# Performance work log

Hardware: AMD Instinct MI355X
Metric: run time of the kernel (lower is better)

Reference implementation:

```python
import jax, jax.numpy as jnp
import numpy as np

B, T, H, K = 128, 4096, 128, 5


def logistic_logcdf(x, mean, log_scale):
    z = (x - mean) * jnp.exp(-log_scale)
    return jax.nn.log_sigmoid(z)


def logistic_logpdf(x, mean, log_scale):
    z = (x - mean) * jnp.exp(-log_scale)
    zh = z / 2
    return -2 * jnp.logaddexp(zh, -zh) - log_scale


def mixlogistic_logcdf(x, prior_logits, means, log_scales):
    x = x[..., None]
    log_pi = jax.nn.log_softmax(prior_logits, axis=-1)
    return jax.nn.logsumexp(log_pi + logistic_logcdf(x, means, log_scales), axis=-1)


def mixlogistic_logpdf(x, prior_logits, means, log_scales):
    x = x[..., None]
    log_pi = jax.nn.log_softmax(prior_logits, axis=-1)
    return jax.nn.logsumexp(log_pi + logistic_logpdf(x, means, log_scales), axis=-1)


def coupling_function(x, pi, mu, log_s):
    log_cdf = jnp.minimum(mixlogistic_logcdf(x, pi, mu, log_s), -1e-12)
    log_1m = jnp.log(-jnp.expm1(log_cdf))
    val = log_cdf - log_1m
    log_jac = mixlogistic_logpdf(x, pi, mu, log_s) - log_cdf - log_1m
    return val, log_jac


def gru_step(h, x, Wi, Wh, bi, bhn):
    # flax GRUCell: input denses have bias, hidden denses no bias except hn.
    gi = x @ Wi + bi                      # [B, 3H]
    gh = h @ Wh                           # [B, 3H]
    ir, iz, inn = jnp.split(gi, 3, axis=-1)
    hr, hz, hn = jnp.split(gh, 3, axis=-1)
    r = jax.nn.sigmoid(ir + hr)
    z = jax.nn.sigmoid(iz + hz)
    n = jnp.tanh(inn + r * (hn + bhn))
    return (1.0 - z) * n + z * h


def setup_inputs() -> dict:
    key = jax.random.key(0)
    ks = jax.random.split(key, 14)
    g = lambda i, shape: (jax.random.normal(ks[i], shape) * 0.08).astype(jnp.float32)
    return {
        's': jax.random.normal(ks[0], (B, T), jnp.float32),
        'x': jax.random.normal(ks[1], (B, T), jnp.float32),
        'eps': jax.random.logistic(ks[2], (B, T), jnp.float32),
        # encoder GRU (in_features=1)
        'Wi_e': g(3, (1, 3 * H)), 'Wh_e': g(4, (H, 3 * H)),
        'bi_e': jnp.zeros(3 * H, jnp.float32), 'bhn_e': jnp.zeros(H, jnp.float32),
        # decoder GRU (in_features=1+H)
        'Wi_d': g(5, (1 + H, 3 * H)), 'Wh_d': g(6, (H, 3 * H)),
        'bi_d': jnp.zeros(3 * H, jnp.float32), 'bhn_d': jnp.zeros(H, jnp.float32),
        # heads
        'W_shift': g(7, (H, 1)), 'b_shift': jnp.zeros(1, jnp.float32),
        'W_lsc': g(8, (H, 1)), 'b_lsc': jnp.zeros(1, jnp.float32),
        'W_pi': g(9, (H, K)), 'b_pi': jnp.zeros(K, jnp.float32),
        'W_mu': g(10, (H, K)), 'b_mu': jnp.zeros(K, jnp.float32),
        'W_ls': g(11, (H, K)), 'b_ls': jnp.zeros(K, jnp.float32),
    }


def reference(s, x, eps, Wi_e, Wh_e, bi_e, bhn_e, Wi_d, Wh_d, bi_d, bhn_d,
              W_shift, b_shift, W_lsc, b_lsc, W_pi, b_pi, W_mu, b_mu, W_ls, b_ls):
    Bn, Tn = s.shape
    Hn = Wh_e.shape[0]
    s3 = s[..., None]  # [B,T,1]
    x3 = x[..., None]

    # --- encoder: reverse GRU, outputs kept in scan (reversed) order ---
    def enc_step(h, xt):
        h = gru_step(h, xt, Wi_e, Wh_e, bi_e, bhn_e)
        return h, h

    x_rev = jnp.flip(x3, axis=1).transpose(1, 0, 2)  # [T,B,1]
    _, h_x = jax.lax.scan(enc_step, jnp.zeros((Bn, Hn), s.dtype), x_rev)
    h_x = h_x.transpose(1, 0, 2)  # [B,T,H]

    sc = jnp.concatenate([s3, h_x], axis=-1)  # [B,T,1+H]

    def dec_step(carry, xs_t):
        h, pred = carry
        inp, e = xs_t              # inp [B,1+H], e [B]
        inp = inp.at[:, 0].set(pred)
        h = gru_step(h, inp, Wi_d, Wh_d, bi_d, bhn_d)
        y = h
        shift = (y @ W_shift + b_shift)[:, 0]
        log_scale = (y @ W_lsc + b_lsc)[:, 0]
        pi = y @ W_pi + b_pi
        mu = y @ W_mu + b_mu
        log_s = y @ W_ls + b_ls
        val, log_jac = coupling_function(e, pi, mu, log_s)
        prediction = shift + val * jnp.exp(log_scale)
        # standard logistic logpdf(e) = -e - 2*softplus(-e)
        logp = (-e - 2 * jax.nn.softplus(-e)) - log_scale - log_jac
        return (h, prediction), (logp, prediction)

    carry0 = (jnp.zeros((Bn, Hn), s.dtype), jnp.zeros(Bn, s.dtype))
    xs = (sc.transpose(1, 0, 2), eps.T)
    _, (logp, preds) = jax.lax.scan(dec_step, carry0, xs)
    return logp.T, preds.T  # each [B,T]
```

## Files before the change

### kernel.cpp

```cpp
#include <hip/hip_runtime.h>
#include <hip/hip_fp16.h>

#define Tn 4096
#define Bn 128
#define Hn 128
#define G3 384
#define NTH 192

typedef unsigned short u16;
typedef unsigned int u32;
typedef _Float16 f16;
typedef _Float16 h2 __attribute__((ext_vector_type(2)));

__device__ __forceinline__ float sigm(float v) { return 1.f / (1.f + __expf(-v)); }
__device__ __forceinline__ float tanh_fast(float v) {
  v = fminf(fmaxf(v, -15.f), 15.f);
  float e = __expf(-2.f * v);
  return (1.f - e) / (1.f + e);
}
__device__ __forceinline__ u16 f2h(float f) { return __half_as_ushort(__float2half(f)); }
__device__ __forceinline__ float h2f(u16 u) { return __half2float(__ushort_as_half(u)); }
__device__ __forceinline__ h2 bch2(u32 v) { union { u32 u; h2 h; } t; t.u = v; return t.h; }
__device__ __forceinline__ float fdot2f(h2 a, h2 b, float c) {
  return __builtin_amdgcn_fdot2(a, b, c, false);
}

__global__ __launch_bounds__(NTH, 1) void combo_kernel(
    const float* __restrict__ x, const float* __restrict__ Wi_e,
    const float* __restrict__ Wh_e, const float* __restrict__ bi_e,
    const float* __restrict__ bhn_e, u16* __restrict__ hx,
    float* __restrict__ enc_h,
    const float* __restrict__ eps, const float* __restrict__ Wi_d,
    const float* __restrict__ Wh_d, const float* __restrict__ bhn_d,
    const float* __restrict__ W_shift, const float* __restrict__ b_shift,
    const float* __restrict__ W_lsc, const float* __restrict__ b_lsc,
    const float* __restrict__ W_pi, const float* __restrict__ b_pi,
    const float* __restrict__ W_mu, const float* __restrict__ b_mu,
    const float* __restrict__ W_ls, const float* __restrict__ b_ls,
    const u16* __restrict__ gi2, float* __restrict__ out,
    float* __restrict__ dec_h, float* __restrict__ dec_pred,
    int enc_t0, int dec_t0, int Tc)
{
  const int j = threadIdx.x;
  __shared__ __align__(16) f16 Xp[2][Hn];
  __shared__ float pred_s;
  const int bid = blockIdx.x;
  int cur = 0;

  if (bid < Bn) {
    if (enc_t0 < 0) return;
    const int b = bid, t0 = enc_t0;
    h2 wr_[64], wz_[64], wn_[64];
    float wieR = 0, wieZ = 0, wieN = 0, bieR = 0, bieZ = 0, bieN = 0;
    float bhn = 0, hm = 0;
    if (j < Hn) {
#pragma unroll
      for (int q = 0; q < 64; ++q) {
        h2 a, bq, c;
        a.x = (f16)Wh_e[(2 * q) * G3 + j];        a.y = (f16)Wh_e[(2 * q + 1) * G3 + j];
        bq.x = (f16)Wh_e[(2 * q) * G3 + 128 + j]; bq.y = (f16)Wh_e[(2 * q + 1) * G3 + 128 + j];
        c.x = (f16)Wh_e[(2 * q) * G3 + 256 + j];  c.y = (f16)Wh_e[(2 * q + 1) * G3 + 256 + j];
        wr_[q] = a; wz_[q] = bq; wn_[q] = c;
      }
      wieR = Wi_e[j]; wieZ = Wi_e[128 + j]; wieN = Wi_e[256 + j];
      bieR = bi_e[j]; bieZ = bi_e[128 + j]; bieN = bi_e[256 + j];
      bhn = bhn_e[j];
      hm = (t0 == 0) ? 0.f : enc_h[(long)b * Hn + j];
      Xp[0][j] = (f16)hm;
    }
    __syncthreads();
    const float* xrow = x + (long)b * Tn;
    u16* hxrow = hx + ((long)b * Hn + (j < Hn ? j : 0)) * Tc;
    for (int i8 = 0; i8 < Tc; i8 += 8) {
      float xc0 = 0, xc1 = 0, xc2 = 0, xc3 = 0, xc4 = 0, xc5 = 0, xc6 = 0, xc7 = 0;
      u32 hb0 = 0, hb1 = 0, hb2 = 0, hb3 = 0;
      if (j < Hn) {
        int base = Tn - 8 - t0 - i8; if (base < 0) base = 0;
        float4 v0 = *(const float4*)(xrow + base);
        float4 v1 = *(const float4*)(xrow + base + 4);
        xc0 = v1.w; xc1 = v1.z; xc2 = v1.y; xc3 = v1.x;
        xc4 = v0.w; xc5 = v0.z; xc6 = v0.y; xc7 = v0.x;
      }
#pragma unroll
      for (int u = 0; u < 8; ++u) {
        if (j < Hn) {
          const uint4* hp = (const uint4*)Xp[cur];
          float a0r = 0, a1r = 0, a0z = 0, a1z = 0, a0n = 0, a1n = 0;
#pragma unroll
          for (int q = 0; q < 16; ++q) {
            uint4 hv = hp[q];
            a0r = fdot2f(bch2(hv.x), wr_[4 * q + 0], a0r);
            a1r = fdot2f(bch2(hv.y), wr_[4 * q + 1], a1r);
            a0r = fdot2f(bch2(hv.z), wr_[4 * q + 2], a0r);
            a1r = fdot2f(bch2(hv.w), wr_[4 * q + 3], a1r);
            a0z = fdot2f(bch2(hv.x), wz_[4 * q + 0], a0z);
            a1z = fdot2f(bch2(hv.y), wz_[4 * q + 1], a1z);
            a0z = fdot2f(bch2(hv.z), wz_[4 * q + 2], a0z);
            a1z = fdot2f(bch2(hv.w), wz_[4 * q + 3], a1z);
            a0n = fdot2f(bch2(hv.x), wn_[4 * q + 0], a0n);
            a1n = fdot2f(bch2(hv.y), wn_[4 * q + 1], a1n);
            a0n = fdot2f(bch2(hv.z), wn_[4 * q + 2], a0n);
            a1n = fdot2f(bch2(hv.w), wn_[4 * q + 3], a1n);
          }
          const float xt = (u == 0) ? xc0 : (u == 1) ? xc1 : (u == 2) ? xc2
                          : (u == 3) ? xc3 : (u == 4) ? xc4 : (u == 5) ? xc5
                          : (u == 6) ? xc6 : xc7;
          float r = sigm((a0r + a1r) + fmaf(xt, wieR, bieR));
          float z = sigm((a0z + a1z) + fmaf(xt, wieZ, bieZ));
          float n = tanh_fast(fmaf(xt, wieN, bieN) + r * ((a0n + a1n) + bhn));
          hm = (1.f - z) * n + z * hm;
          Xp[cur ^ 1][j] = (f16)hm;
          u16 hv16 = f2h(hm);
          if (u == 0) hb0 = hv16; else if (u == 1) hb0 |= ((u32)hv16 << 16);
          else if (u == 2) hb1 = hv16; else if (u == 3) hb1 |= ((u32)hv16 << 16);
          else if (u == 4) hb2 = hv16; else if (u == 5) hb2 |= ((u32)hv16 << 16);
          else if (u == 6) hb3 = hv16; else hb3 |= ((u32)hv16 << 16);
        }
        __syncthreads();
        cur ^= 1;
      }
      if (j < Hn) {
        uint4 o; o.x = hb0; o.y = hb1; o.z = hb2; o.w = hb3;
        *(uint4*)(hxrow + i8) = o;
      }
    }
    if (j < Hn) enc_h[(long)b * Hn + j] = hm;
  } else {
    if (dec_t0 < 0) return;
    const int b = bid - Bn, t0 = dec_t0;
    const int lane = j - 128;
    h2 wr_[64], wz_[64], wn_[64];
    h2 wp2[32];
    float wr0 = 0, wz0 = 0, wn0 = 0, bhn = 0, hm = 0;
    float hbias = 0, predreg = 0;
    if (j < Hn) {
#pragma unroll
      for (int q = 0; q < 64; ++q) {
        h2 a, bq, c;
        a.x = (f16)Wh_d[(2 * q) * G3 + j];        a.y = (f16)Wh_d[(2 * q + 1) * G3 + j];
        bq.x = (f16)Wh_d[(2 * q) * G3 + 128 + j]; bq.y = (f16)Wh_d[(2 * q + 1) * G3 + 128 + j];
        c.x = (f16)Wh_d[(2 * q) * G3 + 256 + j];  c.y = (f16)Wh_d[(2 * q + 1) * G3 + 256 + j];
        wr_[q] = a; wz_[q] = bq; wn_[q] = c;
      }
      wr0 = Wi_d[j]; wz0 = Wi_d[128 + j]; wn0 = Wi_d[256 + j];
      bhn = bhn_d[j];
      hm = (t0 == 0) ? 0.f : dec_h[(long)b * Hn + j];
      Xp[0][j] = (f16)hm;
    } else {
      const int ho = lane >> 1, hs = lane & 1;
      if (lane < 34) {
#pragma unroll
        for (int q = 0; q < 32; ++q) {
          int ka = 2 * (hs * 32 + q), kb = ka + 1;
          float wa, wb;
          if (ho == 0) { wa = W_shift[ka]; wb = W_shift[kb]; }
          else if (ho == 1) { wa = W_lsc[ka]; wb = W_lsc[kb]; }
          else if (ho < 7) { wa = W_pi[ka * 5 + ho - 2]; wb = W_pi[kb * 5 + ho - 2]; }
          else if (ho < 12) { wa = W_mu[ka * 5 + ho - 7]; wb = W_mu[kb * 5 + ho - 7]; }
          else { wa = W_ls[ka * 5 + ho - 12]; wb = W_ls[kb * 5 + ho - 12]; }
          h2 t; t.x = (f16)wa; t.y = (f16)wb;
          wp2[q] = t;
        }
        hbias = (ho == 0) ? b_shift[0] : (ho == 1) ? b_lsc[0] : (ho < 7) ? b_pi[ho - 2]
              : (ho < 12) ? b_mu[ho - 7] : b_ls[ho - 12];
      } else {
#pragma unroll
        for (int q = 0; q < 32; ++q) { h2 t; t.x = (f16)0.f; t.y = (f16)0.f; wp2[q] = t; }
      }
      predreg = (t0 == 0) ? 0.f : dec_pred[b];
      if (lane == 0) pred_s = predreg;
    }
    const float* erow = eps + (long)b * Tn;
    const u16* gibase = gi2 + (long)b * G3 * Tc;
    float ep = 0.f;
    float lp0 = 0, lp1 = 0, lp2 = 0, lp3 = 0, lp4 = 0, lp5 = 0, lp6 = 0, lp7 = 0;
    float pr0 = 0, pr1 = 0, pr2 = 0, pr3 = 0, pr4 = 0, pr5 = 0, pr6 = 0, pr7 = 0;
    float* outlp = out + (long)b * Tn + t0;
    float* outpr = out + (long)Bn * Tn + (long)b * Tn + t0;
    __syncthreads();

    auto couple = [&](float e, const f16* Xc) -> float2 {
      const int hs = lane & 1;
      float p = 0.f;
      if (lane < 34) {
        const uint4* hp4 = (const uint4*)Xc;
#pragma unroll
        for (int q = 0; q < 8; ++q) {
          uint4 hv = hp4[hs * 8 + q];
          p = fdot2f(bch2(hv.x), wp2[4 * q + 0], p);
          p = fdot2f(bch2(hv.y), wp2[4 * q + 1], p);
          p = fdot2f(bch2(hv.z), wp2[4 * q + 2], p);
          p = fdot2f(bch2(hv.w), wp2[4 * q + 3], p);
        }
      }
      p += __shfl_xor(p, 1);
      float pb = p + hbias;
      const int lj2 = lane & 7;
      float pi_ = __shfl(pb, 4 + 2 * lj2);
      float mu_ = __shfl(pb, 14 + 2 * lj2);
      float ls_ = __shfl(pb, 24 + 2 * lj2);
      float shiftv = __shfl(pb, 0);
      float lscv = __shfl(pb, 2);
      const bool valid = (lane < 5);
      float wexp = valid ? __expf(pi_) : 0.f;
      float zz = (e - mu_) * __expf(-ls_);
      float uq = __expf(-fabsf(zz));
      float dq = 1.f / (1.f + uq);
      float sigp = (zz >= 0.f) ? dq : uq * dq;
      float sigq = (zz >= 0.f) ? uq * dq : dq;
      float pdfl = uq * dq * dq * __expf(-ls_);
      float c = wexp * sigp, m = wexp * sigq, pq = wexp * pdfl, S = wexp;
      c += __shfl_xor(c, 1, 8); m += __shfl_xor(m, 1, 8);
      pq += __shfl_xor(pq, 1, 8); S += __shfl_xor(S, 1, 8);
      c += __shfl_xor(c, 2, 8); m += __shfl_xor(m, 2, 8);
      pq += __shfl_xor(pq, 2, 8); S += __shfl_xor(S, 2, 8);
      c += __shfl_xor(c, 4, 8); m += __shfl_xor(m, 4, 8);
      pq += __shfl_xor(pq, 4, 8); S += __shfl_xor(S, 4, 8);
      float logc = __logf(c), logm = __logf(m);
      float val = logc - logm;
      float ljac = __logf(pq) + __logf(S) - logc - logm;
      float prednew = fmaf(val, __expf(lscv), shiftv);
      float sp = fmaxf(-e, 0.f) + log1pf(__expf(-fabsf(e)));
      float logp = (-e - 2.f * sp) - lscv - ljac;
      return make_float2(logp, prednew);
    };

    for (int i8 = 0; i8 < Tc; i8 += 8) {
      uint4 gR4 = {0, 0, 0, 0}, gZ4 = {0, 0, 0, 0}, gN4 = {0, 0, 0, 0};
      float ec0 = 0, ec1 = 0, ec2 = 0, ec3 = 0, ec4 = 0, ec5 = 0, ec6 = 0, ec7 = 0;
      if (j < Hn) {
        gR4 = *(const uint4*)(gibase + (long)j * Tc + i8);
        gZ4 = *(const uint4*)(gibase + (long)(128 + j) * Tc + i8);
        gN4 = *(const uint4*)(gibase + (long)(256 + j) * Tc + i8);
      } else {
        float4 v0 = *(const float4*)(erow + t0 + i8);
        float4 v1 = *(const float4*)(erow + t0 + i8 + 4);
        ec0 = v0.x; ec1 = v0.y; ec2 = v0.z; ec3 = v0.w;
        ec4 = v1.x; ec5 = v1.y; ec6 = v1.z; ec7 = v1.w;
      }
#pragma unroll
      for (int u = 0; u < 8; ++u) {
        const int i = i8 + u;
        float ar = 0, az = 0, an = 0;
        if (j < Hn) {
          const uint4* hp = (const uint4*)Xp[cur];
          float a0r = 0, a1r = 0, a0z = 0, a1z = 0, a0n = 0, a1n = 0;
#pragma unroll
          for (int q = 0; q < 16; ++q) {
            uint4 hv = hp[q];
            a0r = fdot2f(bch2(hv.x), wr_[4 * q + 0], a0r);
            a1r = fdot2f(bch2(hv.y), wr_[4 * q + 1], a1r);
            a0r = fdot2f(bch2(hv.z), wr_[4 * q + 2], a0r);
            a1r = fdot2f(bch2(hv.w), wr_[4 * q + 3], a1r);
            a0z = fdot2f(bch2(hv.x), wz_[4 * q + 0], a0z);
            a1z = fdot2f(bch2(hv.y), wz_[4 * q + 1], a1z);
            a0z = fdot2f(bch2(hv.z), wz_[4 * q + 2], a0z);
            a1z = fdot2f(bch2(hv.w), wz_[4 * q + 3], a1z);
            a0n = fdot2f(bch2(hv.x), wn_[4 * q + 0], a0n);
            a1n = fdot2f(bch2(hv.y), wn_[4 * q + 1], a1n);
            a0n = fdot2f(bch2(hv.z), wn_[4 * q + 2], a0n);
            a1n = fdot2f(bch2(hv.w), wn_[4 * q + 3], a1n);
          }
          ar = a0r + a1r; az = a0z + a1z; an = a0n + a1n;
        } else if (i >= 1) {
          float e = (u == 0) ? ep : (u == 1) ? ec0 : (u == 2) ? ec1 : (u == 3) ? ec2
                  : (u == 4) ? ec3 : (u == 5) ? ec4 : (u == 6) ? ec5 : ec6;
          float2 rr = couple(e, Xp[cur]);
          if (lane == 0) {
            if (u == 0) { lp7 = rr.x; pr7 = rr.y; }
            else if (u == 1) { lp0 = rr.x; pr0 = rr.y; }
            else if (u == 2) { lp1 = rr.x; pr1 = rr.y; }
            else if (u == 3) { lp2 = rr.x; pr2 = rr.y; }
            else if (u == 4) { lp3 = rr.x; pr3 = rr.y; }
            else if (u == 5) { lp4 = rr.x; pr4 = rr.y; }
            else if (u == 6) { lp5 = rr.x; pr5 = rr.y; }
            else { lp6 = rr.x; pr6 = rr.y; }
            pred_s = rr.y;
            predreg = rr.y;
            if (u == 0 && i8 > 0) {
              *(float4*)(outlp + i8 - 8) = make_float4(lp0, lp1, lp2, lp3);
              *(float4*)(outlp + i8 - 4) = make_float4(lp4, lp5, lp6, lp7);
              *(float4*)(outpr + i8 - 8) = make_float4(pr0, pr1, pr2, pr3);
              *(float4*)(outpr + i8 - 4) = make_float4(pr4, pr5, pr6, pr7);
            }
          }
        }
        __syncthreads();
        if (j < Hn) {
          u16 gvr = (u == 0) ? (u16)gR4.x : (u == 1) ? (u16)(gR4.x >> 16)
                  : (u == 2) ? (u16)gR4.y : (u == 3) ? (u16)(gR4.y >> 16)
                  : (u == 4) ? (u16)gR4.z : (u == 5) ? (u16)(gR4.z >> 16)
                  : (u == 6) ? (u16)gR4.w : (u16)(gR4.w >> 16);
          u16 gvz = (u == 0) ? (u16)gZ4.x : (u == 1) ? (u16)(gZ4.x >> 16)
                  : (u == 2) ? (u16)gZ4.y : (u == 3) ? (u16)(gZ4.y >> 16)
                  : (u == 4) ? (u16)gZ4.z : (u == 5) ? (u16)(gZ4.z >> 16)
                  : (u == 6) ? (u16)gZ4.w : (u16)(gZ4.w >> 16);
          u16 gvn = (u == 0) ? (u16)gN4.x : (u == 1) ? (u16)(gN4.x >> 16)
                  : (u == 2) ? (u16)gN4.y : (u == 3) ? (u16)(gN4.y >> 16)
                  : (u == 4) ? (u16)gN4.z : (u == 5) ? (u16)(gN4.z >> 16)
                  : (u == 6) ? (u16)gN4.w : (u16)(gN4.w >> 16);
          float pred = pred_s;
          float r = sigm(ar + h2f(gvr) + pred * wr0);
          float z = sigm(az + h2f(gvz) + pred * wz0);
          float n = tanh_fast(h2f(gvn) + pred * wn0 + r * (an + bhn));
          hm = (1.f - z) * n + z * hm;
          Xp[cur ^ 1][j] = (f16)hm;
        }
        __syncthreads();
        cur ^= 1;
      }
      if (j >= 128) ep = ec7;
    }
    if (j >= 128) {
      float2 rr = couple(ep, Xp[cur]);
      if (lane == 0) {
        lp7 = rr.x; pr7 = rr.y; predreg = rr.y;
        *(float4*)(outlp + Tc - 8) = make_float4(lp0, lp1, lp2, lp3);
        *(float4*)(outlp + Tc - 4) = make_float4(lp4, lp5, lp6, lp7);
        *(float4*)(outpr + Tc - 8) = make_float4(pr0, pr1, pr2, pr3);
        *(float4*)(outpr + Tc - 4) = make_float4(pr4, pr5, pr6, pr7);
      }
    }
    if (j < Hn) dec_h[(long)b * Hn + j] = hm;
    if (j == 128) dec_pred[b] = predreg;
  }
}

__global__ __launch_bounds__(256) void gemm_gi(
    const u16* __restrict__ A2, const float* __restrict__ Wi_d,
    const float* __restrict__ bi_d, u16* __restrict__ C2, int Tc)
{
  __shared__ __align__(16) float As[16][64];
  __shared__ __align__(16) float Ws[16][64];
  const int tid = threadIdx.x;
  const long m0 = (long)blockIdx.x * 64;
  const int n0 = blockIdx.y * 64;
  const int bb = (int)(m0 / Tc);
  const int tt0 = (int)(m0 - (long)bb * Tc);
  const int tx = tid & 15, ty = tid >> 4;
  const int lk = tid >> 4, lm = (tid & 15) * 4;
  const int wk = tid >> 4, wn = (tid & 15) * 4;
  float acc[4][4] = {};
  for (int k0 = 0; k0 < Hn; k0 += 16) {
    uint2 a2v = *(const uint2*)(A2 + ((long)bb * Hn + k0 + lk) * Tc + tt0 + lm);
    float4 w4 = *(const float4*)(Wi_d + (long)(1 + k0 + wk) * G3 + n0 + wn);
    __syncthreads();
    As[lk][lm + 0] = h2f((u16)(a2v.x & 0xffffu));
    As[lk][lm + 1] = h2f((u16)(a2v.x >> 16));
    As[lk][lm + 2] = h2f((u16)(a2v.y & 0xffffu));
    As[lk][lm + 3] = h2f((u16)(a2v.y >> 16));
    *(float4*)&Ws[wk][wn] = w4;
    __syncthreads();
#pragma unroll
    for (int kk = 0; kk < 16; ++kk) {
      float4 av = *(const float4*)&As[kk][ty * 4];
      float4 wv = *(const float4*)&Ws[kk][tx * 4];
      float ar[4] = {av.x, av.y, av.z, av.w};
      float wr[4] = {wv.x, wv.y, wv.z, wv.w};
#pragma unroll
      for (int i = 0; i < 4; ++i)
#pragma unroll
        for (int jj = 0; jj < 4; ++jj) acc[i][jj] = fmaf(ar[i], wr[jj], acc[i][jj]);
    }
  }
  const float4 bbv = *(const float4*)(bi_d + n0 + tx * 4);
  const float br[4] = {bbv.x, bbv.y, bbv.z, bbv.w};
#pragma unroll
  for (int jj = 0; jj < 4; ++jj) {
    int colc = n0 + tx * 4 + jj;
    u32 lo = (u32)f2h(acc[0][jj] + br[jj]) | ((u32)f2h(acc[1][jj] + br[jj]) << 16);
    u32 hi = (u32)f2h(acc[2][jj] + br[jj]) | ((u32)f2h(acc[3][jj] + br[jj]) << 16);
    uint2 o; o.x = lo; o.y = hi;
    *(uint2*)(C2 + ((long)bb * G3 + colc) * Tc + tt0 + ty * 4) = o;
  }
}

extern "C" void kernel_launch(void* const* d_in, const int* in_sizes, int n_in,
                              void* d_out, int out_size, void* d_ws, size_t ws_size,
                              hipStream_t stream) {
  const float* x = (const float*)d_in[1];
  const float* eps = (const float*)d_in[2];
  const float* Wi_e = (const float*)d_in[3];
  const float* Wh_e = (const float*)d_in[4];
  const float* bi_e = (const float*)d_in[5];
  const float* bhn_e = (const float*)d_in[6];
  const float* Wi_d = (const float*)d_in[7];
  const float* Wh_d = (const float*)d_in[8];
  const float* bi_d = (const float*)d_in[9];
  const float* bhn_d = (const float*)d_in[10];
  const float* W_shift = (const float*)d_in[11];
  const float* b_shift = (const float*)d_in[12];
  const float* W_lsc = (const float*)d_in[13];
  const float* b_lsc = (const float*)d_in[14];
  const float* W_pi = (const float*)d_in[15];
  const float* b_pi = (const float*)d_in[16];
  const float* W_mu = (const float*)d_in[17];
  const float* b_mu = (const float*)d_in[18];
  const float* W_ls = (const float*)d_in[19];
  const float* b_ls = (const float*)d_in[20];
  float* out = (float*)d_out;

  const size_t stateB = (size_t)(2 * Bn * Hn + Bn) * sizeof(float);
  const size_t stateAl = (stateB + 255) & ~(size_t)255;
  int Tc = 512;
  while (Tc > 64 && stateAl + (size_t)Bn * Tc * (Hn + G3) * 2 > ws_size) Tc >>= 1;
  if (stateAl + (size_t)Bn * Tc * (Hn + G3) * 2 > ws_size) return;

  float* enc_h = (float*)d_ws;
  float* dec_h = enc_h + (size_t)Bn * Hn;
  float* dec_pred = dec_h + (size_t)Bn * Hn;
  u16* hx = (u16*)((char*)d_ws + stateAl);
  u16* gi = hx + (size_t)Bn * Tc * Hn;

  const int Nc = Tn / Tc;
  const dim3 gg((unsigned)(((size_t)Bn * Tc) / 64), G3 / 64);
  for (int k = 0; k <= Nc; ++k) {
    int enc_t0 = (k < Nc) ? k * Tc : -1;
    int dec_t0 = (k >= 1) ? (k - 1) * Tc : -1;
    combo_kernel<<<2 * Bn, NTH, 0, stream>>>(
        x, Wi_e, Wh_e, bi_e, bhn_e, hx, enc_h,
        eps, Wi_d, Wh_d, bhn_d, W_shift, b_shift, W_lsc, b_lsc,
        W_pi, b_pi, W_mu, b_mu, W_ls, b_ls,
        gi, out, dec_h, dec_pred, enc_t0, dec_t0, Tc);
    if (k < Nc) gemm_gi<<<gg, 256, 0, stream>>>(hx, Wi_d, bi_d, gi, Tc);
  }
}
```

Before: 5.693 ms.

## Split GRU recurrent matvec across an extra wave computing the n-gate

Adds a fourth wavefront per block that computes the candidate-gate (n) hidden matvec and passes it through shared memory, so the main 128 threads handle only the r and z gates. This shortens the serial per-timestep dot-product chain and cuts per-thread weight registers from three gate arrays to two. The head/coupling lane moves to the new fourth wave, and encoder and decoder blocks now share one unified code path. The cost is an extra shared-memory round trip per step and more threads taking part in each barrier.

```diff
diff --git a/kernel.cpp b/kernel.cpp
--- a/kernel.cpp
+++ b/kernel.cpp
@@ -5,7 +5,7 @@
 #define Bn 128
 #define Hn 128
 #define G3 384
-#define NTH 192
+#define NTH 256
 
 typedef unsigned short u16;
 typedef unsigned int u32;
@@ -43,250 +43,232 @@
 {
   const int j = threadIdx.x;
   __shared__ __align__(16) f16 Xp[2][Hn];
+  __shared__ __align__(16) float nds[Hn];
   __shared__ float pred_s;
   const int bid = blockIdx.x;
   int cur = 0;
-
-  if (bid < Bn) {
-    if (enc_t0 < 0) return;
-    const int b = bid, t0 = enc_t0;
-    h2 wr_[64], wz_[64], wn_[64];
-    float wieR = 0, wieZ = 0, wieN = 0, bieR = 0, bieZ = 0, bieN = 0;
-    float bhn = 0, hm = 0;
-    if (j < Hn) {
-#pragma unroll
-      for (int q = 0; q < 64; ++q) {
-        h2 a, bq, c;
-        a.x = (f16)Wh_e[(2 * q) * G3 + j];        a.y = (f16)Wh_e[(2 * q + 1) * G3 + j];
-        bq.x = (f16)Wh_e[(2 * q) * G3 + 128 + j]; bq.y = (f16)Wh_e[(2 * q + 1) * G3 + 128 + j];
-        c.x = (f16)Wh_e[(2 * q) * G3 + 256 + j];  c.y = (f16)Wh_e[(2 * q + 1) * G3 + 256 + j];
-        wr_[q] = a; wz_[q] = bq; wn_[q] = c;
-      }
+  const bool is_enc = bid < Bn;
+  if (is_enc) { if (enc_t0 < 0) return; } else { if (dec_t0 < 0) return; }
+  const int b = is_enc ? bid : bid - Bn;
+  const int t0 = is_enc ? enc_t0 : dec_t0;
+  const float* Wh = is_enc ? Wh_e : Wh_d;
+
+  h2 wa_[64], wb_[64];
+  float hm = 0.f;
+  float bhn = 0, wr0 = 0, wz0 = 0, wn0 = 0;
+  float wieR = 0, wieZ = 0, wieN = 0, bieR = 0, bieZ = 0, bieN = 0;
+  h2 wp2[32];
+  float hbias = 0, predreg = 0;
+
+  if (j < Hn) {
+#pragma unroll
+    for (int q = 0; q < 64; ++q) {
+      h2 a, bq;
+      a.x = (f16)Wh[(2 * q) * G3 + j];        a.y = (f16)Wh[(2 * q + 1) * G3 + j];
+      bq.x = (f16)Wh[(2 * q) * G3 + 128 + j]; bq.y = (f16)Wh[(2 * q + 1) * G3 + 128 + j];
+      wa_[q] = a; wb_[q] = bq;
+    }
+    if (is_enc) {
       wieR = Wi_e[j]; wieZ = Wi_e[128 + j]; wieN = Wi_e[256 + j];
       bieR = bi_e[j]; bieZ = bi_e[128 + j]; bieN = bi_e[256 + j];
       bhn = bhn_e[j];
       hm = (t0 == 0) ? 0.f : enc_h[(long)b * Hn + j];
-      Xp[0][j] = (f16)hm;
-    }
-    __syncthreads();
-    const float* xrow = x + (long)b * Tn;
-    u16* hxrow = hx + ((long)b * Hn + (j < Hn ? j : 0)) * Tc;
-    for (int i8 = 0; i8 < Tc; i8 += 8) {
-      float xc0 = 0, xc1 = 0, xc2 = 0, xc3 = 0, xc4 = 0, xc5 = 0, xc6 = 0, xc7 = 0;
-      u32 hb0 = 0, hb1 = 0, hb2 = 0, hb3 = 0;
-      if (j < Hn) {
+    } else {
+      wr0 = Wi_d[j]; wz0 = Wi_d[128 + j]; wn0 = Wi_d[256 + j];
+      bhn = bhn_d[j];
+      hm = (t0 == 0) ? 0.f : dec_h[(long)b * Hn + j];
+    }
+    Xp[0][j] = (f16)hm;
+  } else if (j < 192) {
+    const int l = j - 128;
+#pragma unroll
+    for (int q = 0; q < 64; ++q) {
+      h2 a, bq;
+      a.x = (f16)Wh[(2 * q) * G3 + 256 + 2 * l];
+      a.y = (f16)Wh[(2 * q + 1) * G3 + 256 + 2 * l];
+      bq.x = (f16)Wh[(2 * q) * G3 + 256 + 2 * l + 1];
+      bq.y = (f16)Wh[(2 * q + 1) * G3 + 256 + 2 * l + 1];
+      wa_[q] = a; wb_[q] = bq;
+    }
+  } else if (!is_enc) {
+    const int lane = j - 192, ho = lane >> 1, hs = lane & 1;
+    if (lane < 34) {
+#pragma unroll
+      for (int q = 0; q < 32; ++q) {
+        int ka = 2 * (hs * 32 + q), kb = ka + 1;
+        float wva, wvb;
+        if (ho == 0) { wva = W_shift[ka]; wvb = W_shift[kb]; }
+        else if (ho == 1) { wva = W_lsc[ka]; wvb = W_lsc[kb]; }
+        else if (ho < 7) { wva = W_pi[ka * 5 + ho - 2]; wvb = W_pi[kb * 5 + ho - 2]; }
+        else if (ho < 12) { wva = W_mu[ka * 5 + ho - 7]; wvb = W_mu[kb * 5 + ho - 7]; }
+        else { wva = W_ls[ka * 5 + ho - 12]; wvb = W_ls[kb * 5 + ho - 12]; }
+        h2 t; t.x = (f16)wva; t.y = (f16)wvb;
+        wp2[q] = t;
+      }
+      hbias = (ho == 0) ? b_shift[0] : (ho == 1) ? b_lsc[0] : (ho < 7) ? b_pi[ho - 2]
+            : (ho < 12) ? b_mu[ho - 7] : b_ls[ho - 12];
+    } else {
+#pragma unroll
+      for (int q = 0; q < 32; ++q) { h2 t; t.x = (f16)0.f; t.y = (f16)0.f; wp2[q] = t; }
+    }
+    predreg = (t0 == 0) ? 0.f : dec_pred[b];
+    if (lane == 0) pred_s = predreg;
+  }
+  __syncthreads();
+
+  const float* xrow = x + (long)b * Tn;
+  const float* erow = eps + (long)b * Tn;
+  const u16* gibase = gi2 + (long)b * G3 * Tc;
+  u16* hxrow = hx + ((long)b * Hn + (j < Hn ? j : 0)) * Tc;
+  float* outlp = out + (long)b * Tn + t0;
+  float* outpr = out + (long)Bn * Tn + (long)b * Tn + t0;
+  const int lane3 = j - 192;
+  float ep = 0.f;
+  float lp0 = 0, lp1 = 0, lp2 = 0, lp3 = 0, lp4 = 0, lp5 = 0, lp6 = 0, lp7 = 0;
+  float pr0 = 0, pr1 = 0, pr2 = 0, pr3 = 0, pr4 = 0, pr5 = 0, pr6 = 0, pr7 = 0;
+
+  auto couple = [&](float e, const f16* Xc) -> float2 {
+    const int hs = lane3 & 1;
+    float p = 0.f;
+    if (lane3 < 34) {
+      const uint4* hp4 = (const uint4*)Xc;
+#pragma unroll
+      for (int q = 0; q < 8; ++q) {
+        uint4 hv = hp4[hs * 8 + q];
+        p = fdot2f(bch2(hv.x), wp2[4 * q + 0], p);
+        p = fdot2f(bch2(hv.y), wp2[4 * q + 1], p);
+        p = fdot2f(bch2(hv.z), wp2[4 * q + 2], p);
+        p = fdot2f(bch2(hv.w), wp2[4 * q + 3], p);
+      }
+    }
+    p += __shfl_xor(p, 1);
+    float pb = p + hbias;
+    const int lj2 = lane3 & 7;
+    float pi_ = __shfl(pb, 4 + 2 * lj2);
+    float mu_ = __shfl(pb, 14 + 2 * lj2);
+    float ls_ = __shfl(pb, 24 + 2 * lj2);
+    float shiftv = __shfl(pb, 0);
+    float lscv = __shfl(pb, 2);
+    const bool valid = (lane3 < 5);
+    float wexp = valid ? __expf(pi_) : 0.f;
+    float zz = (e - mu_) * __expf(-ls_);
+    float uq = __expf(-fabsf(zz));
+    float dq = 1.f / (1.f + uq);
+    float sigp = (zz >= 0.f) ? dq : uq * dq;
+    float sigq = (zz >= 0.f) ? uq * dq : dq;
+    float pdfl = uq * dq * dq * __expf(-ls_);
+    float c = wexp * sigp, m = wexp * sigq, pq = wexp * pdfl, S = wexp;
+    c += __shfl_xor(c, 1, 8); m += __shfl_xor(m, 1, 8);
+    pq += __shfl_xor(pq, 1, 8); S += __shfl_xor(S, 1, 8);
+    c += __shfl_xor(c, 2, 8); m += __shfl_xor(m, 2, 8);
+    pq += __shfl_xor(pq, 2, 8); S += __shfl_xor(S, 2, 8);
+    c += __shfl_xor(c, 4, 8); m += __shfl_xor(m, 4, 8);
+    pq += __shfl_xor(pq, 4, 8); S += __shfl_xor(S, 4, 8);
+    float logc = __logf(c), logm = __logf(m);
+    float val = logc - logm;
+    float ljac = __logf(pq) + __logf(S) - logc - logm;
+    float prednew = fmaf(val, __expf(lscv), shiftv);
+    float sp = fmaxf(-e, 0.f) + log1pf(__expf(-fabsf(e)));
+    float logp = (-e - 2.f * sp) - lscv - ljac;
+    return make_float2(logp, prednew);
+  };
+
+  for (int i8 = 0; i8 < Tc; i8 += 8) {
+    uint4 gR4 = {0, 0, 0, 0}, gZ4 = {0, 0, 0, 0}, gN4 = {0, 0, 0, 0};
+    float xc0 = 0, xc1 = 0, xc2 = 0, xc3 = 0, xc4 = 0, xc5 = 0, xc6 = 0, xc7 = 0;
+    float ec0 = 0, ec1 = 0, ec2 = 0, ec3 = 0, ec4 = 0, ec5 = 0, ec6 = 0, ec7 = 0;
+    u32 hb0 = 0, hb1 = 0, hb2 = 0, hb3 = 0;
+    if (j < Hn) {
+      if (is_enc) {
         int base = Tn - 8 - t0 - i8; if (base < 0) base = 0;
         float4 v0 = *(const float4*)(xrow + base);
         float4 v1 = *(const float4*)(xrow + base + 4);
         xc0 = v1.w; xc1 = v1.z; xc2 = v1.y; xc3 = v1.x;
         xc4 = v0.w; xc5 = v0.z; xc6 = v0.y; xc7 = v0.x;
+      } else {
+        gR4 = *(const uint4*)(gibase + (long)j * Tc + i8);
+        gZ4 = *(const uint4*)(gibase + (long)(128 + j) * Tc + i8);
+        gN4 = *(const uint4*)(gibase + (long)(256 + j) * Tc + i8);
       }
-#pragma unroll
-      for (int u = 0; u < 8; ++u) {
-        if (j < Hn) {
-          const uint4* hp = (const uint4*)Xp[cur];
-          float a0r = 0, a1r = 0, a0z = 0, a1z = 0, a0n = 0, a1n = 0;
-#pragma unroll
-          for (int q = 0; q < 16; ++q) {
-            uint4 hv = hp[q];
-            a0r = fdot2f(bch2(hv.x), wr_[4 * q + 0], a0r);
-            a1r = fdot2f(bch2(hv.y), wr_[4 * q + 1], a1r);
-            a0r = fdot2f(bch2(hv.z), wr_[4 * q + 2], a0r);
-            a1r = fdot2f(bch2(hv.w), wr_[4 * q + 3], a1r);
-            a0z = fdot2f(bch2(hv.x), wz_[4 * q + 0], a0z);
-            a1z = fdot2f(bch2(hv.y), wz_[4 * q + 1], a1z);
-            a0z = fdot2f(bch2(hv.z), wz_[4 * q + 2], a0z);
-            a1z = fdot2f(bch2(hv.w), wz_[4 * q + 3], a1z);
-            a0n = fdot2f(bch2(hv.x), wn_[4 * q + 0], a0n);
-            a1n = fdot2f(bch2(hv.y), wn_[4 * q + 1], a1n);
-            a0n = fdot2f(bch2(hv.z), wn_[4 * q + 2], a0n);
-            a1n = fdot2f(bch2(hv.w), wn_[4 * q + 3], a1n);
+    } else if (j >= 192 && !is_enc) {
+      float4 v0 = *(const float4*)(erow + t0 + i8);
+      float4 v1 = *(const float4*)(erow + t0 + i8 + 4);
+      ec0 = v0.x; ec1 = v0.y; ec2 = v0.z; ec3 = v0.w;
+      ec4 = v1.x; ec5 = v1.y; ec6 = v1.z; ec7 = v1.w;
+    }
+#pragma unroll
+    for (int u = 0; u < 8; ++u) {
+      const int i = i8 + u;
+      float ar = 0, az = 0;
+      if (j < Hn) {
+        const uint4* hp = (const uint4*)Xp[cur];
+        float a0r = 0, a1r = 0, a0z = 0, a1z = 0;
+#pragma unroll
+        for (int q = 0; q < 16; ++q) {
+          uint4 hv = hp[q];
+          a0r = fdot2f(bch2(hv.x), wa_[4 * q + 0], a0r);
+          a1r = fdot2f(bch2(hv.y), wa_[4 * q + 1], a1r);
+          a0r = fdot2f(bch2(hv.z), wa_[4 * q + 2], a0r);
+          a1r = fdot2f(bch2(hv.w), wa_[4 * q + 3], a1r);
+          a0z = fdot2f(bch2(hv.x), wb_[4 * q + 0], a0z);
+          a1z = fdot2f(bch2(hv.y), wb_[4 * q + 1], a1z);
+          a0z = fdot2f(bch2(hv.z), wb_[4 * q + 2], a0z);
+          a1z = fdot2f(bch2(hv.w), wb_[4 * q + 3], a1z);
+        }
+        ar = a0r + a1r; az = a0z + a1z;
+      } else if (j < 192) {
+        const int l = j - 128;
+        const uint4* hp = (const uint4*)Xp[cur];
+        float a0 = 0, a1 = 0, b0 = 0, b1 = 0;
+#pragma unroll
+        for (int q = 0; q < 16; ++q) {
+          uint4 hv = hp[q];
+          a0 = fdot2f(bch2(hv.x), wa_[4 * q + 0], a0);
+          a1 = fdot2f(bch2(hv.y), wa_[4 * q + 1], a1);
+          a0 = fdot2f(bch2(hv.z), wa_[4 * q + 2], a0);
+          a1 = fdot2f(bch2(hv.w), wa_[4 * q + 3], a1);
+          b0 = fdot2f(bch2(hv.x), wb_[4 * q + 0], b0);
+          b1 = fdot2f(bch2(hv.y), wb_[4 * q + 1], b1);
+          b0 = fdot2f(bch2(hv.z), wb_[4 * q + 2], b0);
+          b1 = fdot2f(bch2(hv.w), wb_[4 * q + 3], b1);
+        }
+        float2 nv; nv.x = a0 + a1; nv.y = b0 + b1;
+        *(float2*)&nds[2 * l] = nv;
+      } else if (!is_enc && i >= 1) {
+        float e = (u == 0) ? ep : (u == 1) ? ec0 : (u == 2) ? ec1 : (u == 3) ? ec2
+                : (u == 4) ? ec3 : (u == 5) ? ec4 : (u == 6) ? ec5 : ec6;
+        float2 rr = couple(e, Xp[cur]);
+        if (lane3 == 0) {
+          if (u == 0) { lp7 = rr.x; pr7 = rr.y; }
+          else if (u == 1) { lp0 = rr.x; pr0 = rr.y; }
+          else if (u == 2) { lp1 = rr.x; pr1 = rr.y; }
+          else if (u == 3) { lp2 = rr.x; pr2 = rr.y; }
+          else if (u == 4) { lp3 = rr.x; pr3 = rr.y; }
+          else if (u == 5) { lp4 = rr.x; pr4 = rr.y; }
+          else if (u == 6) { lp5 = rr.x; pr5 = rr.y; }
+          else { lp6 = rr.x; pr6 = rr.y; }
+          pred_s = rr.y;
+          predreg = rr.y;
+          if (u == 0 && i8 > 0) {
+            *(float4*)(outlp + i8 - 8) = make_float4(lp0, lp1, lp2, lp3);
+            *(float4*)(outlp + i8 - 4) = make_float4(lp4, lp5, lp6, lp7);
+            *(float4*)(outpr + i8 - 8) = make_float4(pr0, pr1, pr2, pr3);
+            *(float4*)(outpr + i8 - 4) = make_float4(pr4, pr5, pr6, pr7);
           }
+        }
+      }
+      __syncthreads();
+      if (j < Hn) {
+        float nd = nds[j];
+        float gir, giz, gin;
+        if (is_enc) {
           const float xt = (u == 0) ? xc0 : (u == 1) ? xc1 : (u == 2) ? xc2
                           : (u == 3) ? xc3 : (u == 4) ? xc4 : (u == 5) ? xc5
                           : (u == 6) ? xc6 : xc7;
-          float r = sigm((a0r + a1r) + fmaf(xt, wieR, bieR));
-          float z = sigm((a0z + a1z) + fmaf(xt, wieZ, bieZ));
-          float n = tanh_fast(fmaf(xt, wieN, bieN) + r * ((a0n + a1n) + bhn));
-          hm = (1.f - z) * n + z * hm;
-          Xp[cur ^ 1][j] = (f16)hm;
-          u16 hv16 = f2h(hm);
-          if (u == 0) hb0 = hv16; else if (u == 1) hb0 |= ((u32)hv16 << 16);
-          else if (u == 2) hb1 = hv16; else if (u == 3) hb1 |= ((u32)hv16 << 16);
-          else if (u == 4) hb2 = hv16; else if (u == 5) hb2 |= ((u32)hv16 << 16);
-          else if (u == 6) hb3 = hv16; else hb3 |= ((u32)hv16 << 16);
-        }
-        __syncthreads();
-        cur ^= 1;
-      }
-      if (j < Hn) {
-        uint4 o; o.x = hb0; o.y = hb1; o.z = hb2; o.w = hb3;
-        *(uint4*)(hxrow + i8) = o;
-      }
-    }
-    if (j < Hn) enc_h[(long)b * Hn + j] = hm;
-  } else {
-    if (dec_t0 < 0) return;
-    const int b = bid - Bn, t0 = dec_t0;
-    const int lane = j - 128;
-    h2 wr_[64], wz_[64], wn_[64];
-    h2 wp2[32];
-    float wr0 = 0, wz0 = 0, wn0 = 0, bhn = 0, hm = 0;
-    float hbias = 0, predreg = 0;
-    if (j < Hn) {
-#pragma unroll
-      for (int q = 0; q < 64; ++q) {
-        h2 a, bq, c;
-        a.x = (f16)Wh_d[(2 * q) * G3 + j];        a.y = (f16)Wh_d[(2 * q + 1) * G3 + j];
-        bq.x = (f16)Wh_d[(2 * q) * G3 + 128 + j]; bq.y = (f16)Wh_d[(2 * q + 1) * G3 + 128 + j];
-        c.x = (f16)Wh_d[(2 * q) * G3 + 256 + j];  c.y = (f16)Wh_d[(2 * q + 1) * G3 + 256 + j];
-        wr_[q] = a; wz_[q] = bq; wn_[q] = c;
-      }
-      wr0 = Wi_d[j]; wz0 = Wi_d[128 + j]; wn0 = Wi_d[256 + j];
-      bhn = bhn_d[j];
-      hm = (t0 == 0) ? 0.f : dec_h[(long)b * Hn + j];
-      Xp[0][j] = (f16)hm;
-    } else {
-      const int ho = lane >> 1, hs = lane & 1;
-      if (lane < 34) {
-#pragma unroll
-        for (int q = 0; q < 32; ++q) {
-          int ka = 2 * (hs * 32 + q), kb = ka + 1;
-          float wa, wb;
-          if (ho == 0) { wa = W_shift[ka]; wb = W_shift[kb]; }
-          else if (ho == 1) { wa = W_lsc[ka]; wb = W_lsc[kb]; }
-          else if (ho < 7) { wa = W_pi[ka * 5 + ho - 2]; wb = W_pi[kb * 5 + ho - 2]; }
-          else if (ho < 12) { wa = W_mu[ka * 5 + ho - 7]; wb = W_mu[kb * 5 + ho - 7]; }
-          else { wa = W_ls[ka * 5 + ho - 12]; wb = W_ls[kb * 5 + ho - 12]; }
-          h2 t; t.x = (f16)wa; t.y = (f16)wb;
-          wp2[q] = t;
-        }
-        hbias = (ho == 0) ? b_shift[0] : (ho == 1) ? b_lsc[0] : (ho < 7) ? b_pi[ho - 2]
-              : (ho < 12) ? b_mu[ho - 7] : b_ls[ho - 12];
-      } else {
-#pragma unroll
-        for (int q = 0; q < 32; ++q) { h2 t; t.x = (f16)0.f; t.y = (f16)0.f; wp2[q] = t; }
-      }
-      predreg = (t0 == 0) ? 0.f : dec_pred[b];
-      if (lane == 0) pred_s = predreg;
-    }
-    const float* erow = eps + (long)b * Tn;
-    const u16* gibase = gi2 + (long)b * G3 * Tc;
-    float ep = 0.f;
-    float lp0 = 0, lp1 = 0, lp2 = 0, lp3 = 0, lp4 = 0, lp5 = 0, lp6 = 0, lp7 = 0;
-    float pr0 = 0, pr1 = 0, pr2 = 0, pr3 = 0, pr4 = 0, pr5 = 0, pr6 = 0, pr7 = 0;
-    float* outlp = out + (long)b * Tn + t0;
-    float* outpr = out + (long)Bn * Tn + (long)b * Tn + t0;
-    __syncthreads();
-
-    auto couple = [&](float e, const f16* Xc) -> float2 {
-      const int hs = lane & 1;
-      float p = 0.f;
-      if (lane < 34) {
-        const uint4* hp4 = (const uint4*)Xc;
-#pragma unroll
-        for (int q = 0; q < 8; ++q) {
-          uint4 hv = hp4[hs * 8 + q];
-          p = fdot2f(bch2(hv.x), wp2[4 * q + 0], p);
-          p = fdot2f(bch2(hv.y), wp2[4 * q + 1], p);
-          p = fdot2f(bch2(hv.z), wp2[4 * q + 2], p);
-          p = fdot2f(bch2(hv.w), wp2[4 * q + 3], p);
-        }
-      }
-      p += __shfl_xor(p, 1);
-      float pb = p + hbias;
-      const int lj2 = lane & 7;
-      float pi_ = __shfl(pb, 4 + 2 * lj2);
-      float mu_ = __shfl(pb, 14 + 2 * lj2);
-      float ls_ = __shfl(pb, 24 + 2 * lj2);
-      float shiftv = __shfl(pb, 0);
-      float lscv = __shfl(pb, 2);
-      const bool valid = (lane < 5);
-      float wexp = valid ? __expf(pi_) : 0.f;
-      float zz = (e - mu_) * __expf(-ls_);
-      float uq = __expf(-fabsf(zz));
-      float dq = 1.f / (1.f + uq);
-      float sigp = (zz >= 0.f) ? dq : uq * dq;
-      float sigq = (zz >= 0.f) ? uq * dq : dq;
-      float pdfl = uq * dq * dq * __expf(-ls_);
-      float c = wexp * sigp, m = wexp * sigq, pq = wexp * pdfl, S = wexp;
-      c += __shfl_xor(c, 1, 8); m += __shfl_xor(m, 1, 8);
-      pq += __shfl_xor(pq, 1, 8); S += __shfl_xor(S, 1, 8);
-      c += __shfl_xor(c, 2, 8); m += __shfl_xor(m, 2, 8);
-      pq += __shfl_xor(pq, 2, 8); S += __shfl_xor(S, 2, 8);
-      c += __shfl_xor(c, 4, 8); m += __shfl_xor(m, 4, 8);
-      pq += __shfl_xor(pq, 4, 8); S += __shfl_xor(S, 4, 8);
-      float logc = __logf(c), logm = __logf(m);
-      float val = logc - logm;
-      float ljac = __logf(pq) + __logf(S) - logc - logm;
-      float prednew = fmaf(val, __expf(lscv), shiftv);
-      float sp = fmaxf(-e, 0.f) + log1pf(__expf(-fabsf(e)));
-      float logp = (-e - 2.f * sp) - lscv - ljac;
-      return make_float2(logp, prednew);
-    };
-
-    for (int i8 = 0; i8 < Tc; i8 += 8) {
-      uint4 gR4 = {0, 0, 0, 0}, gZ4 = {0, 0, 0, 0}, gN4 = {0, 0, 0, 0};
-      float ec0 = 0, ec1 = 0, ec2 = 0, ec3 = 0, ec4 = 0, ec5 = 0, ec6 = 0, ec7 = 0;
-      if (j < Hn) {
-        gR4 = *(const uint4*)(gibase + (long)j * Tc + i8);
-        gZ4 = *(const uint4*)(gibase + (long)(128 + j) * Tc + i8);
-        gN4 = *(const uint4*)(gibase + (long)(256 + j) * Tc + i8);
-      } else {
-        float4 v0 = *(const float4*)(erow + t0 + i8);
-        float4 v1 = *(const float4*)(erow + t0 + i8 + 4);
-        ec0 = v0.x; ec1 = v0.y; ec2 = v0.z; ec3 = v0.w;
-        ec4 = v1.x; ec5 = v1.y; ec6 = v1.z; ec7 = v1.w;
-      }
-#pragma unroll
-      for (int u = 0; u < 8; ++u) {
-        const int i = i8 + u;
-        float ar = 0, az = 0, an = 0;
-        if (j < Hn) {
-          const uint4* hp = (const uint4*)Xp[cur];
-          float a0r = 0, a1r = 0, a0z = 0, a1z = 0, a0n = 0, a1n = 0;
-#pragma unroll
-          for (int q = 0; q < 16; ++q) {
-            uint4 hv = hp[q];
-            a0r = fdot2f(bch2(hv.x), wr_[4 * q + 0], a0r);
-            a1r = fdot2f(bch2(hv.y), wr_[4 * q + 1], a1r);
-            a0r = fdot2f(bch2(hv.z), wr_[4 * q + 2], a0r);
-            a1r = fdot2f(bch2(hv.w), wr_[4 * q + 3], a1r);
-            a0z = fdot2f(bch2(hv.x), wz_[4 * q + 0], a0z);
-            a1z = fdot2f(bch2(hv.y), wz_[4 * q + 1], a1z);
-            a0z = fdot2f(bch2(hv.z), wz_[4 * q + 2], a0z);
-            a1z = fdot2f(bch2(hv.w), wz_[4 * q + 3], a1z);
-            a0n = fdot2f(bch2(hv.x), wn_[4 * q + 0], a0n);
-            a1n = fdot2f(bch2(hv.y), wn_[4 * q + 1], a1n);
-            a0n = fdot2f(bch2(hv.z), wn_[4 * q + 2], a0n);
-            a1n = fdot2f(bch2(hv.w), wn_[4 * q + 3], a1n);
-          }
-          ar = a0r + a1r; az = a0z + a1z; an = a0n + a1n;
-        } else if (i >= 1) {
-          float e = (u == 0) ? ep : (u == 1) ? ec0 : (u == 2) ? ec1 : (u == 3) ? ec2
-                  : (u == 4) ? ec3 : (u == 5) ? ec4 : (u == 6) ? ec5 : ec6;
-          float2 rr = couple(e, Xp[cur]);
-          if (lane == 0) {
-            if (u == 0) { lp7 = rr.x; pr7 = rr.y; }
-            else if (u == 1) { lp0 = rr.x; pr0 = rr.y; }
-            else if (u == 2) { lp1 = rr.x; pr1 = rr.y; }
-            else if (u == 3) { lp2 = rr.x; pr2 = rr.y; }
-            else if (u == 4) { lp3 = rr.x; pr3 = rr.y; }
-            else if (u == 5) { lp4 = rr.x; pr4 = rr.y; }
-            else if (u == 6) { lp5 = rr.x; pr5 = rr.y; }
-            else { lp6 = rr.x; pr6 = rr.y; }
-            pred_s = rr.y;
-            predreg = rr.y;
-            if (u == 0 && i8 > 0) {
-              *(float4*)(outlp + i8 - 8) = make_float4(lp0, lp1, lp2, lp3);
-              *(float4*)(outlp + i8 - 4) = make_float4(lp4, lp5, lp6, lp7);
-              *(float4*)(outpr + i8 - 8) = make_float4(pr0, pr1, pr2, pr3);
-              *(float4*)(outpr + i8 - 4) = make_float4(pr4, pr5, pr6, pr7);
-            }
-          }
-        }
-        __syncthreads();
-        if (j < Hn) {
+          gir = fmaf(xt, wieR, bieR);
+          giz = fmaf(xt, wieZ, bieZ);
+          gin = fmaf(xt, wieN, bieN);
+        } else {
           u16 gvr = (u == 0) ? (u16)gR4.x : (u == 1) ? (u16)(gR4.x >> 16)
                   : (u == 2) ? (u16)gR4.y : (u == 3) ? (u16)(gR4.y >> 16)
                   : (u == 4) ? (u16)gR4.z : (u == 5) ? (u16)(gR4.z >> 16)
@@ -300,30 +282,44 @@
                   : (u == 4) ? (u16)gN4.z : (u == 5) ? (u16)(gN4.z >> 16)
                   : (u == 6) ? (u16)gN4.w : (u16)(gN4.w >> 16);
           float pred = pred_s;
-          float r = sigm(ar + h2f(gvr) + pred * wr0);
-          float z = sigm(az + h2f(gvz) + pred * wz0);
-          float n = tanh_fast(h2f(gvn) + pred * wn0 + r * (an + bhn));
-          hm = (1.f - z) * n + z * hm;
-          Xp[cur ^ 1][j] = (f16)hm;
+          gir = h2f(gvr) + pred * wr0;
+          giz = h2f(gvz) + pred * wz0;
+          gin = h2f(gvn) + pred * wn0;
         }
-        __syncthreads();
-        cur ^= 1;
+        float r = sigm(ar + gir);
+        float z = sigm(az + giz);
+        float n = tanh_fast(gin + r * (nd + bhn));
+        hm = (1.f - z) * n + z * hm;
+        Xp[cur ^ 1][j] = (f16)hm;
+        if (is_enc) {
+          u16 hv16 = f2h(hm);
+          if (u == 0) hb0 = hv16; else if (u == 1) hb0 |= ((u32)hv16 << 16);
+          else if (u == 2) hb1 = hv16; else if (u == 3) hb1 |= ((u32)hv16 << 16);
+          else if (u == 4) hb2 = hv16; else if (u == 5) hb2 |= ((u32)hv16 << 16);
+          else if (u == 6) hb3 = hv16; else hb3 |= ((u32)hv16 << 16);
+        }
       }
-      if (j >= 128) ep = ec7;
-    }
-    if (j >= 128) {
-      float2 rr = couple(ep, Xp[cur]);
-      if (lane == 0) {
-        lp7 = rr.x; pr7 = rr.y; predreg = rr.y;
-        *(float4*)(outlp + Tc - 8) = make_float4(lp0, lp1, lp2, lp3);
-        *(float4*)(outlp + Tc - 4) = make_float4(lp4, lp5, lp6, lp7);
-        *(float4*)(outpr + Tc - 8) = make_float4(pr0, pr1, pr2, pr3);
-        *(float4*)(outpr + Tc - 4) = make_float4(pr4, pr5, pr6, pr7);
-      }
-    }
-    if (j < Hn) dec_h[(long)b * Hn + j] = hm;
-    if (j == 128) dec_pred[b] = predreg;
-  }
+      __syncthreads();
+      cur ^= 1;
+    }
+    if (is_enc && j < Hn) {
+      uint4 o; o.x = hb0; o.y = hb1; o.z = hb2; o.w = hb3;
+      *(uint4*)(hxrow + i8) = o;
+    }
+    if (!is_enc && j >= 192) ep = ec7;
+  }
+  if (!is_enc && j >= 192) {
+    float2 rr = couple(ep, Xp[cur]);
+    if (lane3 == 0) {
+      lp7 = rr.x; pr7 = rr.y; predreg = rr.y;
+      *(float4*)(outlp + Tc - 8) = make_float4(lp0, lp1, lp2, lp3);
+      *(float4*)(outlp + Tc - 4) = make_float4(lp4, lp5, lp6, lp7);
+      *(float4*)(outpr + Tc - 8) = make_float4(pr0, pr1, pr2, pr3);
+      *(float4*)(outpr + Tc - 4) = make_float4(pr4, pr5, pr6, pr7);
+    }
+  }
+  if (j < Hn) (is_enc ? enc_h : dec_h)[(long)b * Hn + j] = hm;
+  if (!is_enc && j == 192) dec_pred[b] = predreg;
 }
 
 __global__ __launch_bounds__(256) void gemm_gi(
```

Result: no change. 5.623 ms (-1.2%).
